# Kernel tuning notes

Measured on AMD Instinct MI355X. Metric: run time of the kernel, lower is better.

The kernel has to match this reference:

```python
import jax, jax.numpy as jnp
import numpy as np

EPS = 1e-9  # projective normalization epsilon
LN_EPS = 1e-5


def setup_inputs() -> dict:
    N, E, Fin, Fout = 50000, 600000, 128, 128
    key = jax.random.key(0)
    ks = jax.random.split(key, 8)
    x = jax.random.normal(ks[0], (N, Fin), jnp.float32)
    edge_index = jax.random.randint(ks[1], (2, E), 0, N, dtype=jnp.int64)
    edge_weight = jax.random.normal(ks[2], (E,), jnp.float32)
    W_self = jax.random.normal(ks[3], (Fin, Fout), jnp.float32) / np.sqrt(Fin)
    b_self = jnp.zeros((Fout,), jnp.float32)
    W_nb = jax.random.normal(ks[4], (Fin, Fout), jnp.float32) / np.sqrt(Fin)
    b_nb = jnp.zeros((Fout,), jnp.float32)
    gamma = jnp.ones((Fout,), jnp.float32)
    beta = jnp.zeros((Fout,), jnp.float32)
    return dict(x=x, edge_index=edge_index, edge_weight=edge_weight,
                W_self=W_self, b_self=b_self, W_nb=W_nb, b_nb=b_nb,
                gamma=gamma, beta=beta)


def _proj_normalize(v):
    # UHG projective_average tail: L2-normalize the weighted sum
    return v / (jnp.linalg.norm(v, axis=-1, keepdims=True) + EPS)


def reference(x, edge_index, edge_weight, W_self, b_self, W_nb, b_nb, gamma, beta):
    N = x.shape[0]
    src, tgt = edge_index[0], edge_index[1]

    # --- neighbor aggregation: per-target softmax over edge weights, then
    # weighted projective average of gathered source features (vectorized
    # replacement of the per-node python loop) ---
    seg_max = jax.ops.segment_max(edge_weight, tgt, num_segments=N)  # [N]
    ew = jnp.exp(edge_weight - seg_max[tgt])                          # [E]
    denom = jax.ops.segment_sum(ew, tgt, num_segments=N)              # [N]
    alpha = ew / denom[tgt]                                           # softmax per target
    agg = jax.ops.segment_sum(alpha[:, None] * x[src], tgt, num_segments=N)  # [N, Fin]
    agg = _proj_normalize(agg)  # isolated nodes stay exactly zero (0 / eps)

    # --- self / neighbor linear transforms ---
    self_feat = x @ W_self + b_self    # [N, Fout]
    nb_feat = agg @ W_nb + b_nb        # [N, Fout]

    # --- combine: projective average with weights [0.5, 0.5] ---
    comb = _proj_normalize(0.5 * (self_feat + nb_feat))

    # --- UHG layer norm (standard layernorm over feature dim) ---
    mu = jnp.mean(comb, axis=-1, keepdims=True)
    var = jnp.var(comb, axis=-1, keepdims=True)
    out = (comb - mu) / jnp.sqrt(var + LN_EPS) * gamma + beta
    # dropout is identity in eval mode
    return out
```

## Files before the change

kernel.cpp:

```cpp
#include <hip/hip_runtime.h>
#include <hip/hip_bf16.h>
#include <hip/hip_fp16.h>

#define EPS 1e-9f
#define LN_EPS 1e-5f

typedef __attribute__((ext_vector_type(8))) short bf16x8;
typedef __attribute__((ext_vector_type(4))) float f32x4;

__device__ __forceinline__ float lo16(unsigned p) { return __uint_as_float(p << 16); }
__device__ __forceinline__ float hi16(unsigned p) { return __uint_as_float(p & 0xffff0000u); }
__device__ __forceinline__ unsigned f2b(float f) {
    unsigned u = __float_as_uint(f);
    return (u + 0x7fffu + ((u >> 16) & 1u)) >> 16;
}
__device__ __forceinline__ int eidx(const int* ei, int i, int i64) {
    return i64 ? ei[2 * i] : ei[i];
}
__device__ __forceinline__ float ldw(const float* fp, const __hip_bfloat16* hp, int i, int f32) {
    return f32 ? fp[i] : __bfloat162float(hp[i]);
}

__global__ void probe_kernel(const unsigned* __restrict__ xb, const int* __restrict__ ei,
                             int* __restrict__ flags) {
    int lane = threadIdx.x & 63;
    unsigned d = xb[lane * 97];
    unsigned ex = (d >> 7) & 0xFFu;
    unsigned long long m1 = __ballot(ex >= 110u && ex <= 135u);
    int hi = ei[2 * lane + 1];
    unsigned long long m2 = __ballot(hi == 0);
    if (lane == 0) {
        flags[0] = (__popcll(m1) > 32) ? 0 : 1;
        flags[1] = (__popcll(m2) > 32) ? 1 : 0;
    }
}

__global__ void prep(const float4* __restrict__ xf4, uint2* __restrict__ xcvt2,
                     const unsigned* __restrict__ Wsb, const float* __restrict__ Wsf,
                     const unsigned* __restrict__ Wnb, const float* __restrict__ Wnf,
                     unsigned* __restrict__ wt, const int* __restrict__ flags, int n4) {
    if (blockIdx.x < 64) {
        int tid = blockIdx.x * 256 + threadIdx.x;
        int f = tid >> 7, k2 = tid & 127;
        int k2l = k2 & 63;
        unsigned out;
        if (flags[0]) {
            const float* W = (k2 < 64) ? Wsf : Wnf;
            float lo = W[(2 * k2l) * 128 + f], hi = W[(2 * k2l + 1) * 128 + f];
            out = f2b(lo) | (f2b(hi) << 16);
        } else {
            const unsigned* W = (k2 < 64) ? Wsb : Wnb;
            unsigned lo = W[(2 * k2l) * 64 + (f >> 1)];
            unsigned hi = W[(2 * k2l + 1) * 64 + (f >> 1)];
            unsigned a = (f & 1) ? (lo >> 16) : (lo & 0xffffu);
            unsigned b = (f & 1) ? (hi & 0xffff0000u) : (hi << 16);
            out = a | b;
        }
        wt[tid] = out;
    } else {
        if (!flags[0]) return;
        int i = (blockIdx.x - 64) * 256 + threadIdx.x;
        if (i >= n4) return;
        float4 v = xf4[i];
        xcvt2[i] = make_uint2(f2b(v.x) | (f2b(v.y) << 16), f2b(v.z) | (f2b(v.w) << 16));
    }
}

__global__ void edge_count(const int* __restrict__ ei, int* __restrict__ count,
                           int* __restrict__ tgt32, int* __restrict__ rank,
                           const int* __restrict__ flags, int E) {
    int e0 = (blockIdx.x * 256 + threadIdx.x) * 4;
    if (e0 >= E) return;
    int i64 = flags[1];
    if (e0 + 4 <= E) {
        int t0 = eidx(ei, E + e0 + 0, i64), t1 = eidx(ei, E + e0 + 1, i64),
            t2 = eidx(ei, E + e0 + 2, i64), t3 = eidx(ei, E + e0 + 3, i64);
        int r0 = atomicAdd(&count[t0], 1), r1 = atomicAdd(&count[t1], 1),
            r2 = atomicAdd(&count[t2], 1), r3 = atomicAdd(&count[t3], 1);
        *(int4*)(tgt32 + e0) = make_int4(t0, t1, t2, t3);
        *(int4*)(rank + e0)  = make_int4(r0, r1, r2, r3);
    } else {
        for (int j = 0; j < 4 && e0 + j < E; ++j) {
            int t = eidx(ei, E + e0 + j, i64);
            rank[e0 + j] = atomicAdd(&count[t], 1);
            tgt32[e0 + j] = t;
        }
    }
}

__global__ void scan_blocks(const int* __restrict__ count, int* __restrict__ offsets,
                            int* __restrict__ bsum, int N) {
    __shared__ int wsum[16];
    int tid = threadIdx.x, lane = tid & 63, w = tid >> 6;
    int i0 = blockIdx.x * 4096 + tid * 4;
    int4 v;
    if (i0 + 3 < N) v = *(const int4*)(count + i0);
    else {
        v.x = (i0     < N) ? count[i0]     : 0;
        v.y = (i0 + 1 < N) ? count[i0 + 1] : 0;
        v.z = (i0 + 2 < N) ? count[i0 + 2] : 0;
        v.w = (i0 + 3 < N) ? count[i0 + 3] : 0;
    }
    int s = v.x + v.y + v.z + v.w;
    int incl = s;
    #pragma unroll
    for (int off = 1; off < 64; off <<= 1) {
        int t = __shfl_up(incl, off);
        if (lane >= off) incl += t;
    }
    if (lane == 63) wsum[w] = incl;
    __syncthreads();
    int wpre = 0, tot = 0;
    #pragma unroll
    for (int j = 0; j < 16; ++j) { int sj = wsum[j]; if (j < w) wpre += sj; tot += sj; }
    int o0 = wpre + incl - s;
    int o1 = o0 + v.x, o2 = o1 + v.y, o3 = o2 + v.z;
    if (i0 + 3 < N) {
        *(int4*)(offsets + i0) = make_int4(o0, o1, o2, o3);
    } else {
        if (i0     < N) offsets[i0]     = o0;
        if (i0 + 1 < N) offsets[i0 + 1] = o1;
        if (i0 + 2 < N) offsets[i0 + 2] = o2;
    }
    if (tid == 0) bsum[blockIdx.x] = tot;
}

__global__ void scan_fixup(int* __restrict__ offsets, const int* __restrict__ bsum,
                           int N, int B) {
    __shared__ int s_pre;
    int b = blockIdx.x;
    if (threadIdx.x == 0) {
        int p = 0;
        for (int j = 0; j < b; ++j) p += bsum[j];
        s_pre = p;
        if (b == B - 1) {
            int tot = p;
            for (int j = b; j < B; ++j) tot += bsum[j];
            offsets[N] = tot;
        }
    }
    __syncthreads();
    int pre = s_pre;
    if (pre == 0) return;
    int i0 = b * 4096 + threadIdx.x * 4;
    if (i0 + 3 < N) {
        int4 t = *(int4*)(offsets + i0);
        t.x += pre; t.y += pre; t.z += pre; t.w += pre;
        *(int4*)(offsets + i0) = t;
    } else {
        for (int j = 0; j < 4; ++j)
            if (i0 + j < N) offsets[i0 + j] += pre;
    }
}

template <int PACK>
__global__ void edge_scatter(const int* __restrict__ ei, const int* __restrict__ tgt32,
                             const int* __restrict__ rank,
                             const float* __restrict__ ewf, const __hip_bfloat16* __restrict__ ewh,
                             const int* __restrict__ offsets, unsigned* __restrict__ csr4,
                             uint2* __restrict__ csr8, const int* __restrict__ flags, int E) {
    int e0 = (blockIdx.x * 256 + threadIdx.x) * 4;
    if (e0 >= E) return;
    int f32 = flags[0], i64 = flags[1];
    if (e0 + 4 <= E) {
        int4 t = *(const int4*)(tgt32 + e0);
        int4 r = *(const int4*)(rank + e0);
        int s0 = eidx(ei, e0 + 0, i64), s1 = eidx(ei, e0 + 1, i64),
            s2 = eidx(ei, e0 + 2, i64), s3 = eidx(ei, e0 + 3, i64);
        float w0 = ldw(ewf, ewh, e0 + 0, f32), w1 = ldw(ewf, ewh, e0 + 1, f32),
              w2 = ldw(ewf, ewh, e0 + 2, f32), w3 = ldw(ewf, ewh, e0 + 3, f32);
        int o0 = offsets[t.x] + r.x, o1 = offsets[t.y] + r.y,
            o2 = offsets[t.z] + r.z, o3 = offsets[t.w] + r.w;
        float a0 = expf(w0), a1 = expf(w1), a2 = expf(w2), a3 = expf(w3);
        if (PACK) {
            csr4[o0] = (unsigned)s0 | ((unsigned)__half_as_ushort(__float2half(a0)) << 16);
            csr4[o1] = (unsigned)s1 | ((unsigned)__half_as_ushort(__float2half(a1)) << 16);
            csr4[o2] = (unsigned)s2 | ((unsigned)__half_as_ushort(__float2half(a2)) << 16);
            csr4[o3] = (unsigned)s3 | ((unsigned)__half_as_ushort(__float2half(a3)) << 16);
        } else {
            csr8[o0] = make_uint2((unsigned)s0, __float_as_uint(a0));
            csr8[o1] = make_uint2((unsigned)s1, __float_as_uint(a1));
            csr8[o2] = make_uint2((unsigned)s2, __float_as_uint(a2));
            csr8[o3] = make_uint2((unsigned)s3, __float_as_uint(a3));
        }
    } else {
        for (int j = 0; j < 4 && e0 + j < E; ++j) {
            int e = e0 + j;
            int t = tgt32[e];
            int s = eidx(ei, e, i64);
            float al = expf(ldw(ewf, ewh, e, f32));
            int pos = offsets[t] + rank[e];
            if (PACK) csr4[pos] = (unsigned)s | ((unsigned)__half_as_ushort(__float2half(al)) << 16);
            else      csr8[pos] = make_uint2((unsigned)s, __float_as_uint(al));
        }
    }
}

template <int PACK>
__device__ __forceinline__ void dec_edge(const unsigned* __restrict__ c4,
                                         const uint2* __restrict__ c8, int j,
                                         unsigned& s, float& al) {
    if (PACK) {
        unsigned r = c4[j];
        s = r & 0xffffu;
        al = __half2float(__ushort_as_half((unsigned short)(r >> 16)));
    } else {
        uint2 e = c8[j];
        s = e.x;
        al = __uint_as_float(e.y);
    }
}

template <int PACK>
__global__ void aggregate(const unsigned* __restrict__ xb, const unsigned* __restrict__ xcvt,
                          const int* __restrict__ offsets, const unsigned* __restrict__ csr4,
                          const uint2* __restrict__ csr8, unsigned* __restrict__ aggb,
                          const int* __restrict__ flags, int N) {
    int node = blockIdx.x * 4 + (threadIdx.x >> 6);
    if (node >= N) return;
    int lane = threadIdx.x & 63;
    const unsigned* xs = flags[0] ? xcvt : xb;
    float a0 = 0.f, a1 = 0.f;
    int beg = offsets[node], end = offsets[node + 1];
    int j = beg;
    for (; j + 8 <= end; j += 8) {
        unsigned s0, s1, s2, s3, s4, s5, s6, s7;
        float l0, l1, l2, l3, l4, l5, l6, l7;
        dec_edge<PACK>(csr4, csr8, j+0, s0, l0); dec_edge<PACK>(csr4, csr8, j+1, s1, l1);
        dec_edge<PACK>(csr4, csr8, j+2, s2, l2); dec_edge<PACK>(csr4, csr8, j+3, s3, l3);
        dec_edge<PACK>(csr4, csr8, j+4, s4, l4); dec_edge<PACK>(csr4, csr8, j+5, s5, l5);
        dec_edge<PACK>(csr4, csr8, j+6, s6, l6); dec_edge<PACK>(csr4, csr8, j+7, s7, l7);
        unsigned p0 = xs[s0 * 64 + lane], p1 = xs[s1 * 64 + lane],
                 p2 = xs[s2 * 64 + lane], p3 = xs[s3 * 64 + lane],
                 p4 = xs[s4 * 64 + lane], p5 = xs[s5 * 64 + lane],
                 p6 = xs[s6 * 64 + lane], p7 = xs[s7 * 64 + lane];
        a0 += l0 * lo16(p0); a1 += l0 * hi16(p0);
        a0 += l1 * lo16(p1); a1 += l1 * hi16(p1);
        a0 += l2 * lo16(p2); a1 += l2 * hi16(p2);
        a0 += l3 * lo16(p3); a1 += l3 * hi16(p3);
        a0 += l4 * lo16(p4); a1 += l4 * hi16(p4);
        a0 += l5 * lo16(p5); a1 += l5 * hi16(p5);
        a0 += l6 * lo16(p6); a1 += l6 * hi16(p6);
        a0 += l7 * lo16(p7); a1 += l7 * hi16(p7);
    }
    for (; j + 4 <= end; j += 4) {
        unsigned s0, s1, s2, s3;
        float l0, l1, l2, l3;
        dec_edge<PACK>(csr4, csr8, j+0, s0, l0); dec_edge<PACK>(csr4, csr8, j+1, s1, l1);
        dec_edge<PACK>(csr4, csr8, j+2, s2, l2); dec_edge<PACK>(csr4, csr8, j+3, s3, l3);
        unsigned p0 = xs[s0 * 64 + lane], p1 = xs[s1 * 64 + lane],
                 p2 = xs[s2 * 64 + lane], p3 = xs[s3 * 64 + lane];
        a0 += l0 * lo16(p0); a1 += l0 * hi16(p0);
        a0 += l1 * lo16(p1); a1 += l1 * hi16(p1);
        a0 += l2 * lo16(p2); a1 += l2 * hi16(p2);
        a0 += l3 * lo16(p3); a1 += l3 * hi16(p3);
    }
    for (; j < end; ++j) {
        unsigned s; float l;
        dec_edge<PACK>(csr4, csr8, j, s, l);
        unsigned p = xs[s * 64 + lane];
        a0 += l * lo16(p); a1 += l * hi16(p);
    }
    float ss = a0 * a0 + a1 * a1;
    #pragma unroll
    for (int m = 32; m >= 1; m >>= 1) ss += __shfl_xor(ss, m);
    float inv = 1.f / (sqrtf(ss) + EPS);
    aggb[node * 64 + lane] = f2b(a0 * inv) | (f2b(a1 * inv) << 16);
}

__global__ __launch_bounds__(128) void fused_mfma(
    const unsigned* __restrict__ xb, const unsigned* __restrict__ xcvt,
    const unsigned* __restrict__ aggb, const uint4* __restrict__ wt4,
    const float* __restrict__ bsf, const __hip_bfloat16* __restrict__ bsh,
    const float* __restrict__ bnf, const __hip_bfloat16* __restrict__ bnh,
    const float* __restrict__ gf, const __hip_bfloat16* __restrict__ gh,
    const float* __restrict__ tf, const __hip_bfloat16* __restrict__ th,
    float* __restrict__ outf, unsigned* __restrict__ outb,
    const int* __restrict__ flags, int N)
{
    __shared__ uint4 sA[1024];
    int f32 = flags[0];
    const uint4* xs4 = (const uint4*)(f32 ? xcvt : xb);
    const uint4* ag4 = (const uint4*)aggb;
    int tid = threadIdx.x;
    int node0 = blockIdx.x * 32;

    #pragma unroll
    for (int i = 0; i < 8; ++i) {
        int ci = i * 128 + tid;
        int r = ci >> 5, c = ci & 31;
        int node = node0 + r;
        uint4 v = make_uint4(0, 0, 0, 0);
        if (node < N) v = (c < 16) ? xs4[node * 16 + c] : ag4[node * 16 + (c - 16)];
        sA[r * 32 + (c ^ (r & 15))] = v;
    }
    __syncthreads();

    int lane = tid & 63, w = tid >> 6, g = lane >> 4, c16 = lane & 15;
    int rloc = w * 16 + c16;

    f32x4 acc[8];
    #pragma unroll
    for (int t = 0; t < 8; ++t) acc[t] = (f32x4){0.f, 0.f, 0.f, 0.f};

    #pragma unroll
    for (int kk = 0; kk < 8; ++kk) {
        uint4 av = sA[rloc * 32 + ((kk * 4 + g) ^ c16)];
        bf16x8 a = __builtin_bit_cast(bf16x8, av);
        #pragma unroll
        for (int t = 0; t < 8; ++t) {
            uint4 bv = wt4[(t * 16 + c16) * 32 + kk * 4 + g];
            bf16x8 b = __builtin_bit_cast(bf16x8, bv);
            acc[t] = __builtin_amdgcn_mfma_f32_16x16x32_bf16(a, b, acc[t], 0, 0, 0);
        }
    }

    float bsum[8], gam[8], bet[8];
    #pragma unroll
    for (int t = 0; t < 8; ++t) {
        int f = t * 16 + c16;
        bsum[t] = ldw(bsf, bsh, f, f32) + ldw(bnf, bnh, f, f32);
        gam[t]  = ldw(gf, gh, f, f32);
        bet[t]  = ldw(tf, th, f, f32);
    }

    #pragma unroll
    for (int reg = 0; reg < 4; ++reg) {
        int node = node0 + w * 16 + g * 4 + reg;
        float cv[8], s1 = 0.f, s2 = 0.f;
        #pragma unroll
        for (int t = 0; t < 8; ++t) {
            float c_ = 0.5f * (acc[t][reg] + bsum[t]);
            cv[t] = c_; s1 += c_; s2 += c_ * c_;
        }
        #pragma unroll
        for (int m = 1; m < 16; m <<= 1) { s1 += __shfl_xor(s1, m); s2 += __shfl_xor(s2, m); }
        float inv  = 1.f / (sqrtf(s2) + EPS);
        float mean = s1 * inv * (1.f / 128.f);
        float var  = s2 * inv * inv * (1.f / 128.f) - mean * mean;
        float rstd = 1.f / sqrtf(var + LN_EPS);
        if (f32) {
            if (node < N) {
                #pragma unroll
                for (int t = 0; t < 8; ++t) {
                    float o = (cv[t] * inv - mean) * rstd * gam[t] + bet[t];
                    outf[(size_t)node * 128 + t * 16 + c16] = o;
                }
            }
        } else {
            #pragma unroll
            for (int t = 0; t < 8; ++t) {
                float o = (cv[t] * inv - mean) * rstd * gam[t] + bet[t];
                float po = __shfl_xor(o, 1);
                if (!(c16 & 1) && node < N)
                    outb[node * 64 + t * 8 + (c16 >> 1)] = f2b(o) | (f2b(po) << 16);
            }
        }
    }
}

static inline size_t rup16(size_t x) { return (x + 15) & ~(size_t)15; }

extern "C" void kernel_launch(void* const* d_in, const int* in_sizes, int n_in,
                              void* d_out, int out_size, void* d_ws, size_t ws_size,
                              hipStream_t stream) {
    int N = in_sizes[0] / 128;
    int E = in_sizes[1] / 2;
    const int* ei = (const int*)d_in[1];

    char* p = (char*)d_ws;
    int* flags = (int*)p;              p += 16;
    int* count = (int*)p;              p += rup16((size_t)N * 4);
    int* offsets = (int*)p;            p += rup16((size_t)(N + 4) * 4);
    int* bsum = (int*)p;               p += 256;
    int* tgt32 = (int*)p;              p += rup16((size_t)E * 4);
    int* rank = (int*)p;               p += rup16((size_t)E * 4);
    unsigned* csr4 = (unsigned*)p;
    uint2* csr8 = (uint2*)p;           p += rup16((size_t)E * 8);
    unsigned* wt = (unsigned*)p;       p += 128 * 128 * 4;
    unsigned* xcvt = (unsigned*)p;     p += rup16((size_t)N * 64 * 4);
    unsigned* aggb = (unsigned*)p;

    hipMemsetAsync(d_ws, 0, 16 + (size_t)N * 4, stream);

    int eb4 = (E + 1023) / 1024;
    int nb = (N + 3) / 4;
    int nbf = (N + 31) / 32;
    int ncv = (N * 32 + 255) / 256;
    int scanB = (N + 4095) / 4096;
    int pack = (N <= 65536);

    probe_kernel<<<1, 64, 0, stream>>>((const unsigned*)d_in[0], ei, flags);
    prep<<<64 + ncv, 256, 0, stream>>>((const float4*)d_in[0], (uint2*)xcvt,
                                       (const unsigned*)d_in[3], (const float*)d_in[3],
                                       (const unsigned*)d_in[5], (const float*)d_in[5],
                                       wt, flags, N * 32);
    edge_count<<<eb4, 256, 0, stream>>>(ei, count, tgt32, rank, flags, E);
    scan_blocks<<<scanB, 1024, 0, stream>>>(count, offsets, bsum, N);
    scan_fixup<<<scanB, 1024, 0, stream>>>(offsets, bsum, N, scanB);
    if (pack)
        edge_scatter<1><<<eb4, 256, 0, stream>>>(ei, tgt32, rank, (const float*)d_in[2],
                                                 (const __hip_bfloat16*)d_in[2],
                                                 offsets, csr4, csr8, flags, E);
    else
        edge_scatter<0><<<eb4, 256, 0, stream>>>(ei, tgt32, rank, (const float*)d_in[2],
                                                 (const __hip_bfloat16*)d_in[2],
                                                 offsets, csr4, csr8, flags, E);
    if (pack)
        aggregate<1><<<nb, 256, 0, stream>>>((const unsigned*)d_in[0], xcvt,
                                             offsets, csr4, csr8, aggb, flags, N);
    else
        aggregate<0><<<nb, 256, 0, stream>>>((const unsigned*)d_in[0], xcvt,
                                             offsets, csr4, csr8, aggb, flags, N);
    fused_mfma<<<nbf, 128, 0, stream>>>((const unsigned*)d_in[0], xcvt, aggb, (const uint4*)wt,
                                        (const float*)d_in[4], (const __hip_bfloat16*)d_in[4],
                                        (const float*)d_in[6], (const __hip_bfloat16*)d_in[6],
                                        (const float*)d_in[7], (const __hip_bfloat16*)d_in[7],
                                        (const float*)d_in[8], (const __hip_bfloat16*)d_in[8],
                                        (float*)d_out, (unsigned*)d_out, flags, N);
}
```

Before: 209.1 us.

## Fuse neighbor aggregation into MFMA kernel and fold count memset into prep

Merges the aggregation kernel into the MFMA projection kernel. Each 128-thread block now aggregates its 32 nodes into shared memory before the matmul, which removes the bf16 agg buffer round trip through global memory and one launch. The count zeroing moves from hipMemsetAsync into extra prep blocks, and edge index loads are vectorized. In exchange, the fused kernel has only 2 waves per block doing the latency-bound gathers serially over 16 nodes each, so it may expose less parallelism than the old 4-node-per-block aggregate.

```diff
diff --git a/kernel.cpp b/kernel.cpp
--- a/kernel.cpp
+++ b/kernel.cpp
@@ -14,7 +14,7 @@
     unsigned u = __float_as_uint(f);
     return (u + 0x7fffu + ((u >> 16) & 1u)) >> 16;
 }
-__device__ __forceinline__ int eidx(const int* ei, int i, int i64) {
+__device__ __forceinline__ int eidx(const int* ei, size_t i, int i64) {
     return i64 ? ei[2 * i] : ei[i];
 }
 __device__ __forceinline__ float ldw(const float* fp, const __hip_bfloat16* hp, int i, int f32) {
@@ -38,9 +38,11 @@
 __global__ void prep(const float4* __restrict__ xf4, uint2* __restrict__ xcvt2,
                      const unsigned* __restrict__ Wsb, const float* __restrict__ Wsf,
                      const unsigned* __restrict__ Wnb, const float* __restrict__ Wnf,
-                     unsigned* __restrict__ wt, const int* __restrict__ flags, int n4) {
-    if (blockIdx.x < 64) {
-        int tid = blockIdx.x * 256 + threadIdx.x;
+                     unsigned* __restrict__ wt, int4* __restrict__ count4,
+                     const int* __restrict__ flags, int n4, int zb, int N4z) {
+    int b = blockIdx.x;
+    if (b < 64) {
+        int tid = b * 256 + threadIdx.x;
         int f = tid >> 7, k2 = tid & 127;
         int k2l = k2 & 63;
         unsigned out;
@@ -53,13 +55,16 @@
             unsigned lo = W[(2 * k2l) * 64 + (f >> 1)];
             unsigned hi = W[(2 * k2l + 1) * 64 + (f >> 1)];
             unsigned a = (f & 1) ? (lo >> 16) : (lo & 0xffffu);
-            unsigned b = (f & 1) ? (hi & 0xffff0000u) : (hi << 16);
-            out = a | b;
+            unsigned b2 = (f & 1) ? (hi & 0xffff0000u) : (hi << 16);
+            out = a | b2;
         }
         wt[tid] = out;
+    } else if (b < 64 + zb) {
+        int i = (b - 64) * 256 + threadIdx.x;
+        if (i < N4z) count4[i] = make_int4(0, 0, 0, 0);
     } else {
         if (!flags[0]) return;
-        int i = (blockIdx.x - 64) * 256 + threadIdx.x;
+        int i = (b - 64 - zb) * 256 + threadIdx.x;
         if (i >= n4) return;
         float4 v = xf4[i];
         xcvt2[i] = make_uint2(f2b(v.x) | (f2b(v.y) << 16), f2b(v.z) | (f2b(v.w) << 16));
@@ -73,15 +78,25 @@
     if (e0 >= E) return;
     int i64 = flags[1];
     if (e0 + 4 <= E) {
-        int t0 = eidx(ei, E + e0 + 0, i64), t1 = eidx(ei, E + e0 + 1, i64),
-            t2 = eidx(ei, E + e0 + 2, i64), t3 = eidx(ei, E + e0 + 3, i64);
+        int t0, t1, t2, t3;
+        if (i64 && !(E & 1)) {
+            const int4* q = (const int4*)(ei + 2 * (size_t)(E + e0));
+            int4 a = q[0], b = q[1];
+            t0 = a.x; t1 = a.z; t2 = b.x; t3 = b.z;
+        } else if (!i64 && !(E & 3)) {
+            int4 a = *(const int4*)(ei + (size_t)E + e0);
+            t0 = a.x; t1 = a.y; t2 = a.z; t3 = a.w;
+        } else {
+            t0 = eidx(ei, (size_t)E + e0 + 0, i64); t1 = eidx(ei, (size_t)E + e0 + 1, i64);
+            t2 = eidx(ei, (size_t)E + e0 + 2, i64); t3 = eidx(ei, (size_t)E + e0 + 3, i64);
+        }
         int r0 = atomicAdd(&count[t0], 1), r1 = atomicAdd(&count[t1], 1),
             r2 = atomicAdd(&count[t2], 1), r3 = atomicAdd(&count[t3], 1);
         *(int4*)(tgt32 + e0) = make_int4(t0, t1, t2, t3);
         *(int4*)(rank + e0)  = make_int4(r0, r1, r2, r3);
     } else {
         for (int j = 0; j < 4 && e0 + j < E; ++j) {
-            int t = eidx(ei, E + e0 + j, i64);
+            int t = eidx(ei, (size_t)E + e0 + j, i64);
             rank[e0 + j] = atomicAdd(&count[t], 1);
             tgt32[e0 + j] = t;
         }
@@ -165,8 +180,17 @@
     if (e0 + 4 <= E) {
         int4 t = *(const int4*)(tgt32 + e0);
         int4 r = *(const int4*)(rank + e0);
-        int s0 = eidx(ei, e0 + 0, i64), s1 = eidx(ei, e0 + 1, i64),
-            s2 = eidx(ei, e0 + 2, i64), s3 = eidx(ei, e0 + 3, i64);
+        int s0, s1, s2, s3;
+        if (i64) {
+            const int4* q = (const int4*)(ei + 2 * (size_t)e0);
+            int4 a = q[0], b = q[1];
+            s0 = a.x; s1 = a.z; s2 = b.x; s3 = b.z;
+        } else if (!(e0 & 3)) {
+            int4 a = *(const int4*)(ei + e0);
+            s0 = a.x; s1 = a.y; s2 = a.z; s3 = a.w;
+        } else {
+            s0 = ei[e0]; s1 = ei[e0 + 1]; s2 = ei[e0 + 2]; s3 = ei[e0 + 3];
+        }
         float w0 = ldw(ewf, ewh, e0 + 0, f32), w1 = ldw(ewf, ewh, e0 + 1, f32),
               w2 = ldw(ewf, ewh, e0 + 2, f32), w3 = ldw(ewf, ewh, e0 + 3, f32);
         int o0 = offsets[t.x] + r.x, o1 = offsets[t.y] + r.y,
@@ -212,65 +236,10 @@
 }
 
 template <int PACK>
-__global__ void aggregate(const unsigned* __restrict__ xb, const unsigned* __restrict__ xcvt,
-                          const int* __restrict__ offsets, const unsigned* __restrict__ csr4,
-                          const uint2* __restrict__ csr8, unsigned* __restrict__ aggb,
-                          const int* __restrict__ flags, int N) {
-    int node = blockIdx.x * 4 + (threadIdx.x >> 6);
-    if (node >= N) return;
-    int lane = threadIdx.x & 63;
-    const unsigned* xs = flags[0] ? xcvt : xb;
-    float a0 = 0.f, a1 = 0.f;
-    int beg = offsets[node], end = offsets[node + 1];
-    int j = beg;
-    for (; j + 8 <= end; j += 8) {
-        unsigned s0, s1, s2, s3, s4, s5, s6, s7;
-        float l0, l1, l2, l3, l4, l5, l6, l7;
-        dec_edge<PACK>(csr4, csr8, j+0, s0, l0); dec_edge<PACK>(csr4, csr8, j+1, s1, l1);
-        dec_edge<PACK>(csr4, csr8, j+2, s2, l2); dec_edge<PACK>(csr4, csr8, j+3, s3, l3);
-        dec_edge<PACK>(csr4, csr8, j+4, s4, l4); dec_edge<PACK>(csr4, csr8, j+5, s5, l5);
-        dec_edge<PACK>(csr4, csr8, j+6, s6, l6); dec_edge<PACK>(csr4, csr8, j+7, s7, l7);
-        unsigned p0 = xs[s0 * 64 + lane], p1 = xs[s1 * 64 + lane],
-                 p2 = xs[s2 * 64 + lane], p3 = xs[s3 * 64 + lane],
-                 p4 = xs[s4 * 64 + lane], p5 = xs[s5 * 64 + lane],
-                 p6 = xs[s6 * 64 + lane], p7 = xs[s7 * 64 + lane];
-        a0 += l0 * lo16(p0); a1 += l0 * hi16(p0);
-        a0 += l1 * lo16(p1); a1 += l1 * hi16(p1);
-        a0 += l2 * lo16(p2); a1 += l2 * hi16(p2);
-        a0 += l3 * lo16(p3); a1 += l3 * hi16(p3);
-        a0 += l4 * lo16(p4); a1 += l4 * hi16(p4);
-        a0 += l5 * lo16(p5); a1 += l5 * hi16(p5);
-        a0 += l6 * lo16(p6); a1 += l6 * hi16(p6);
-        a0 += l7 * lo16(p7); a1 += l7 * hi16(p7);
-    }
-    for (; j + 4 <= end; j += 4) {
-        unsigned s0, s1, s2, s3;
-        float l0, l1, l2, l3;
-        dec_edge<PACK>(csr4, csr8, j+0, s0, l0); dec_edge<PACK>(csr4, csr8, j+1, s1, l1);
-        dec_edge<PACK>(csr4, csr8, j+2, s2, l2); dec_edge<PACK>(csr4, csr8, j+3, s3, l3);
-        unsigned p0 = xs[s0 * 64 + lane], p1 = xs[s1 * 64 + lane],
-                 p2 = xs[s2 * 64 + lane], p3 = xs[s3 * 64 + lane];
-        a0 += l0 * lo16(p0); a1 += l0 * hi16(p0);
-        a0 += l1 * lo16(p1); a1 += l1 * hi16(p1);
-        a0 += l2 * lo16(p2); a1 += l2 * hi16(p2);
-        a0 += l3 * lo16(p3); a1 += l3 * hi16(p3);
-    }
-    for (; j < end; ++j) {
-        unsigned s; float l;
-        dec_edge<PACK>(csr4, csr8, j, s, l);
-        unsigned p = xs[s * 64 + lane];
-        a0 += l * lo16(p); a1 += l * hi16(p);
-    }
-    float ss = a0 * a0 + a1 * a1;
-    #pragma unroll
-    for (int m = 32; m >= 1; m >>= 1) ss += __shfl_xor(ss, m);
-    float inv = 1.f / (sqrtf(ss) + EPS);
-    aggb[node * 64 + lane] = f2b(a0 * inv) | (f2b(a1 * inv) << 16);
-}
-
-__global__ __launch_bounds__(128) void fused_mfma(
+__global__ __launch_bounds__(128) void agg_mfma(
     const unsigned* __restrict__ xb, const unsigned* __restrict__ xcvt,
-    const unsigned* __restrict__ aggb, const uint4* __restrict__ wt4,
+    const int* __restrict__ offsets, const unsigned* __restrict__ csr4,
+    const uint2* __restrict__ csr8, const uint4* __restrict__ wt4,
     const float* __restrict__ bsf, const __hip_bfloat16* __restrict__ bsh,
     const float* __restrict__ bnf, const __hip_bfloat16* __restrict__ bnh,
     const float* __restrict__ gf, const __hip_bfloat16* __restrict__ gh,
@@ -278,26 +247,81 @@
     float* __restrict__ outf, unsigned* __restrict__ outb,
     const int* __restrict__ flags, int N)
 {
-    __shared__ uint4 sA[1024];
+    __shared__ uint4 sX[32 * 16];
+    __shared__ unsigned sG[32 * 64];
     int f32 = flags[0];
-    const uint4* xs4 = (const uint4*)(f32 ? xcvt : xb);
-    const uint4* ag4 = (const uint4*)aggb;
-    int tid = threadIdx.x;
+    const unsigned* xs = f32 ? xcvt : xb;
+    const uint4* xs4 = (const uint4*)xs;
+    int tid = threadIdx.x, lane = tid & 63, w = tid >> 6;
     int node0 = blockIdx.x * 32;
 
     #pragma unroll
-    for (int i = 0; i < 8; ++i) {
+    for (int i = 0; i < 4; ++i) {
         int ci = i * 128 + tid;
-        int r = ci >> 5, c = ci & 31;
+        int r = ci >> 4, c = ci & 15;
         int node = node0 + r;
         uint4 v = make_uint4(0, 0, 0, 0);
-        if (node < N) v = (c < 16) ? xs4[node * 16 + c] : ag4[node * 16 + (c - 16)];
-        sA[r * 32 + (c ^ (r & 15))] = v;
+        if (node < N) v = xs4[node * 16 + c];
+        sX[r * 16 + (c ^ (r & 15))] = v;
+    }
+
+    int cg = lane >> 2, sub = lane & 3;
+    for (int i = 0; i < 16; ++i) {
+        int r = w * 16 + i;
+        int node = node0 + r;
+        float a0 = 0.f, a1 = 0.f;
+        int beg = 0, end = 0;
+        if (node < N) { beg = offsets[node]; end = offsets[node + 1]; }
+        int j = beg;
+        for (; j + 8 <= end; j += 8) {
+            unsigned s0, s1, s2, s3, s4, s5, s6, s7;
+            float l0, l1, l2, l3, l4, l5, l6, l7;
+            dec_edge<PACK>(csr4, csr8, j+0, s0, l0); dec_edge<PACK>(csr4, csr8, j+1, s1, l1);
+            dec_edge<PACK>(csr4, csr8, j+2, s2, l2); dec_edge<PACK>(csr4, csr8, j+3, s3, l3);
+            dec_edge<PACK>(csr4, csr8, j+4, s4, l4); dec_edge<PACK>(csr4, csr8, j+5, s5, l5);
+            dec_edge<PACK>(csr4, csr8, j+6, s6, l6); dec_edge<PACK>(csr4, csr8, j+7, s7, l7);
+            unsigned p0 = xs[s0 * 64 + lane], p1 = xs[s1 * 64 + lane],
+                     p2 = xs[s2 * 64 + lane], p3 = xs[s3 * 64 + lane],
+                     p4 = xs[s4 * 64 + lane], p5 = xs[s5 * 64 + lane],
+                     p6 = xs[s6 * 64 + lane], p7 = xs[s7 * 64 + lane];
+            a0 += l0 * lo16(p0); a1 += l0 * hi16(p0);
+            a0 += l1 * lo16(p1); a1 += l1 * hi16(p1);
+            a0 += l2 * lo16(p2); a1 += l2 * hi16(p2);
+            a0 += l3 * lo16(p3); a1 += l3 * hi16(p3);
+            a0 += l4 * lo16(p4); a1 += l4 * hi16(p4);
+            a0 += l5 * lo16(p5); a1 += l5 * hi16(p5);
+            a0 += l6 * lo16(p6); a1 += l6 * hi16(p6);
+            a0 += l7 * lo16(p7); a1 += l7 * hi16(p7);
+        }
+        for (; j + 4 <= end; j += 4) {
+            unsigned s0, s1, s2, s3;
+            float l0, l1, l2, l3;
+            dec_edge<PACK>(csr4, csr8, j+0, s0, l0); dec_edge<PACK>(csr4, csr8, j+1, s1, l1);
+            dec_edge<PACK>(csr4, csr8, j+2, s2, l2); dec_edge<PACK>(csr4, csr8, j+3, s3, l3);
+            unsigned p0 = xs[s0 * 64 + lane], p1 = xs[s1 * 64 + lane],
+                     p2 = xs[s2 * 64 + lane], p3 = xs[s3 * 64 + lane];
+            a0 += l0 * lo16(p0); a1 += l0 * hi16(p0);
+            a0 += l1 * lo16(p1); a1 += l1 * hi16(p1);
+            a0 += l2 * lo16(p2); a1 += l2 * hi16(p2);
+            a0 += l3 * lo16(p3); a1 += l3 * hi16(p3);
+        }
+        for (; j < end; ++j) {
+            unsigned s; float l;
+            dec_edge<PACK>(csr4, csr8, j, s, l);
+            unsigned p = xs[s * 64 + lane];
+            a0 += l * lo16(p); a1 += l * hi16(p);
+        }
+        float ss = a0 * a0 + a1 * a1;
+        #pragma unroll
+        for (int m = 32; m >= 1; m >>= 1) ss += __shfl_xor(ss, m);
+        float inv = 1.f / (sqrtf(ss) + EPS);
+        sG[r * 64 + ((cg ^ (r & 15)) << 2) + sub] = f2b(a0 * inv) | (f2b(a1 * inv) << 16);
     }
     __syncthreads();
 
-    int lane = tid & 63, w = tid >> 6, g = lane >> 4, c16 = lane & 15;
+    int g = lane >> 4, c16 = lane & 15;
     int rloc = w * 16 + c16;
+    const uint4* sG4 = (const uint4*)sG;
 
     f32x4 acc[8];
     #pragma unroll
@@ -305,7 +329,9 @@
 
     #pragma unroll
     for (int kk = 0; kk < 8; ++kk) {
-        uint4 av = sA[rloc * 32 + ((kk * 4 + g) ^ c16)];
+        int c = kk * 4 + g;
+        uint4 av = (kk < 4) ? sX[rloc * 16 + (c ^ c16)]
+                            : sG4[rloc * 16 + ((c - 16) ^ c16)];
         bf16x8 a = __builtin_bit_cast(bf16x8, av);
         #pragma unroll
         for (int t = 0; t < 8; ++t) {
@@ -378,23 +404,21 @@
     unsigned* csr4 = (unsigned*)p;
     uint2* csr8 = (uint2*)p;           p += rup16((size_t)E * 8);
     unsigned* wt = (unsigned*)p;       p += 128 * 128 * 4;
-    unsigned* xcvt = (unsigned*)p;     p += rup16((size_t)N * 64 * 4);
-    unsigned* aggb = (unsigned*)p;
-
-    hipMemsetAsync(d_ws, 0, 16 + (size_t)N * 4, stream);
+    unsigned* xcvt = (unsigned*)p;
 
     int eb4 = (E + 1023) / 1024;
-    int nb = (N + 3) / 4;
     int nbf = (N + 31) / 32;
     int ncv = (N * 32 + 255) / 256;
     int scanB = (N + 4095) / 4096;
+    int N4z = (int)(rup16((size_t)N * 4) / 16);
+    int zb = (N4z + 255) / 256;
     int pack = (N <= 65536);
 
     probe_kernel<<<1, 64, 0, stream>>>((const unsigned*)d_in[0], ei, flags);
-    prep<<<64 + ncv, 256, 0, stream>>>((const float4*)d_in[0], (uint2*)xcvt,
-                                       (const unsigned*)d_in[3], (const float*)d_in[3],
-                                       (const unsigned*)d_in[5], (const float*)d_in[5],
-                                       wt, flags, N * 32);
+    prep<<<64 + zb + ncv, 256, 0, stream>>>((const float4*)d_in[0], (uint2*)xcvt,
+                                            (const unsigned*)d_in[3], (const float*)d_in[3],
+                                            (const unsigned*)d_in[5], (const float*)d_in[5],
+                                            wt, (int4*)count, flags, N * 32, zb, N4z);
     edge_count<<<eb4, 256, 0, stream>>>(ei, count, tgt32, rank, flags, E);
     scan_blocks<<<scanB, 1024, 0, stream>>>(count, offsets, bsum, N);
     scan_fixup<<<scanB, 1024, 0, stream>>>(offsets, bsum, N, scanB);
@@ -407,15 +431,19 @@
                                                  (const __hip_bfloat16*)d_in[2],
                                                  offsets, csr4, csr8, flags, E);
     if (pack)
-        aggregate<1><<<nb, 256, 0, stream>>>((const unsigned*)d_in[0], xcvt,
-                                             offsets, csr4, csr8, aggb, flags, N);
+        agg_mfma<1><<<nbf, 128, 0, stream>>>((const unsigned*)d_in[0], xcvt, offsets, csr4, csr8,
+                                             (const uint4*)wt,
+                                             (const float*)d_in[4], (const __hip_bfloat16*)d_in[4],
+                                             (const float*)d_in[6], (const __hip_bfloat16*)d_in[6],
+                                             (const float*)d_in[7], (const __hip_bfloat16*)d_in[7],
+                                             (const float*)d_in[8], (const __hip_bfloat16*)d_in[8],
+                                             (float*)d_out, (unsigned*)d_out, flags, N);
     else
-        aggregate<0><<<nb, 256, 0, stream>>>((const unsigned*)d_in[0], xcvt,
-                                             offsets, csr4, csr8, aggb, flags, N);
-    fused_mfma<<<nbf, 128, 0, stream>>>((const unsigned*)d_in[0], xcvt, aggb, (const uint4*)wt,
-                                        (const float*)d_in[4], (const __hip_bfloat16*)d_in[4],
-                                        (const float*)d_in[6], (const __hip_bfloat16*)d_in[6],
-                                        (const float*)d_in[7], (const __hip_bfloat16*)d_in[7],
-                                        (const float*)d_in[8], (const __hip_bfloat16*)d_in[8],
-                                        (float*)d_out, (unsigned*)d_out, flags, N);
-}
+        agg_mfma<0><<<nbf, 128, 0, stream>>>((const unsigned*)d_in[0], xcvt, offsets, csr4, csr8,
+                                             (const uint4*)wt,
+                                             (const float*)d_in[4], (const __hip_bfloat16*)d_in[4],
+                                             (const float*)d_in[6], (const __hip_bfloat16*)d_in[6],
+                                             (const float*)d_in[7], (const __hip_bfloat16*)d_in[7],
+                                             (const float*)d_in[8], (const __hip_bfloat16*)d_in[8],
+                                             (float*)d_out, (unsigned*)d_out, flags, N);
+}
```

Measured after the change: 242.0 us. +15.7%, slower.
